# Kernel tuning notes

Hardware: AMD Instinct MI355X
Metric: run time of the kernel (lower is better)

## Reference

```python
import jax, jax.numpy as jnp
import numpy as np

D_MODEL = 1024
NUM_HEADS = 16
D_K = D_MODEL // NUM_HEADS


def setup_inputs() -> dict:
    key = jax.random.key(0)
    ks = jax.random.split(key, 5)
    x = jax.random.normal(ks[0], (8, 1024, D_MODEL), dtype=jnp.float32)
    s_in = 1.0 / np.sqrt(D_MODEL)
    W_qkv = jax.random.normal(ks[1], (D_MODEL, 3 * D_MODEL), dtype=jnp.float32) * s_in
    b_qkv = jax.random.normal(ks[2], (3 * D_MODEL,), dtype=jnp.float32) * 0.01
    W_o = jax.random.normal(ks[3], (D_MODEL, D_MODEL), dtype=jnp.float32) * s_in
    b_o = jax.random.normal(ks[4], (D_MODEL,), dtype=jnp.float32) * 0.01
    return {"x": x, "W_qkv": W_qkv, "b_qkv": b_qkv, "W_o": W_o, "b_o": b_o}


def reference(x, W_qkv, b_qkv, W_o, b_o):
    B, N, D = x.shape
    qkv = x @ W_qkv + b_qkv                      # [B, N, 3D]
    qkv = qkv.reshape(B, N, 3, NUM_HEADS, D_K)
    qkv = jnp.transpose(qkv, (2, 0, 3, 1, 4))    # [3, B, H, N, d_k]
    q, k, v = qkv[0], qkv[1], qkv[2]
    scale = 1.0 / np.sqrt(D_K).astype(np.float32)
    attn = jnp.einsum('bhqd,bhkd->bhqk', q, k) * scale
    attn = jax.nn.softmax(attn, axis=-1)
    out = jnp.einsum('bhqk,bhkd->bhqd', attn, v)  # [B, H, N, d_k]
    out = jnp.transpose(out, (0, 2, 1, 3)).reshape(B, N, D)
    return out @ W_o + b_o
```

## Files before the change

kernel.cpp:

```cpp
#include <hip/hip_runtime.h>


typedef __attribute__((ext_vector_type(8))) short bf16x8;
typedef __attribute__((ext_vector_type(4))) float f32x4;

#define GLOAD_LDS16(gp, lp)                                                              \
  __builtin_amdgcn_global_load_lds((const __attribute__((address_space(1))) void*)(gp),  \
                                   (__attribute__((address_space(3))) void*)(lp), 16, 0, 0)

__device__ __forceinline__ unsigned short f2bf(float f) {
  unsigned int u = __float_as_uint(f);
  u += 0x7fffu + ((u >> 16) & 1u);
  return (unsigned short)(u >> 16);
}

__global__ __launch_bounds__(256) void prep_fused(
    const float* __restrict__ x, unsigned short* __restrict__ x_bf,
    const float* __restrict__ W_qkv, unsigned short* __restrict__ wqkv_t,
    const float* __restrict__ W_o, unsigned short* __restrict__ wo_t) {
  const int b = blockIdx.x;
  if (b < 2048) {
    const int n4 = 8388608 / 4;
    for (int i = b * 256 + threadIdx.x; i < n4; i += 2048 * 256) {
      float4 v = reinterpret_cast<const float4*>(x)[i];
      ushort4 o;
      o.x = f2bf(v.x); o.y = f2bf(v.y); o.z = f2bf(v.z); o.w = f2bf(v.w);
      reinterpret_cast<ushort4*>(x_bf)[i] = o;
    }
  } else {
    __shared__ float tile[32][33];
    const float* W;
    unsigned short* Wt;
    int R = 1024, C, bx, by;
    if (b < 5120) {
      W = W_qkv; Wt = wqkv_t; C = 3072;
      int bb = b - 2048; bx = bb % 96; by = bb / 96;
    } else {
      W = W_o; Wt = wo_t; C = 1024;
      int bb = b - 5120; bx = bb & 31; by = bb >> 5;
    }
    const int tx = threadIdx.x & 31, ty = threadIdx.x >> 5;
    const int c0 = bx * 32, r0 = by * 32;
    #pragma unroll
    for (int i = 0; i < 4; i++) {
      int r = r0 + ty + i * 8;
      tile[ty + i * 8][tx] = W[(size_t)r * C + c0 + tx];
    }
    __syncthreads();
    #pragma unroll
    for (int i = 0; i < 4; i++) {
      int c = c0 + ty + i * 8;
      Wt[(size_t)c * R + r0 + tx] = f2bf(tile[tx][ty + i * 8]);
    }
  }
}

__global__ __launch_bounds__(512) void gemm1_384(
    const unsigned short* __restrict__ A, const unsigned short* __restrict__ Bt,
    const float* __restrict__ bias, unsigned short* __restrict__ qkv_out) {
  __shared__ __align__(16) unsigned short As[3][128 * 32];
  __shared__ __align__(16) unsigned short Bs[3][384 * 32];
  const int t = threadIdx.x;
  const int lane = t & 63, wid = t >> 6;
  const int lr = lane & 15, g = lane >> 4;
  const int wm = wid >> 2, wn = wid & 3;

  const int nwg = gridDim.x * gridDim.y;
  const int id = blockIdx.x + gridDim.x * blockIdx.y;
  const int sw = (id & 7) * (nwg >> 3) + (id >> 3);
  const int bx = sw % gridDim.x, by = sw / gridDim.x;
  const int row0 = by * 128, col0 = bx * 384;

  const int srow = t >> 2;
  const int sch  = (t & 3) ^ ((srow >> 1) & 3);

  auto stA = [&](int buf, int kt) {
    GLOAD_LDS16(A + (size_t)(row0 + srow) * 1024 + kt * 32 + sch * 8,
                (char*)&As[buf][0] + t * 16);
  };
  auto stB = [&](int buf, int kt, int j) {
    GLOAD_LDS16(Bt + (size_t)(col0 + j * 128 + srow) * 1024 + kt * 32 + sch * 8,
                (char*)&Bs[buf][0] + j * 8192 + t * 16);
  };
  auto rdA = [&](int buf, int m) -> bf16x8 {
    int r = wm * 64 + m * 16 + lr;
    return *(const bf16x8*)((const char*)&As[buf][0] + r * 64 +
                            ((g ^ ((r >> 1) & 3)) * 16));
  };
  auto rdB = [&](int buf, int n) -> bf16x8 {
    int r = wn * 96 + n * 16 + lr;
    return *(const bf16x8*)((const char*)&Bs[buf][0] + r * 64 +
                            ((g ^ ((r >> 1) & 3)) * 16));
  };

  f32x4 acc[4][6] = {};

  stA(0, 0); stB(0, 0, 0); stB(0, 0, 1); stB(0, 0, 2);
  stA(1, 1); stB(1, 1, 0); stB(1, 1, 1); stB(1, 1, 2);

  for (int kt = 0; kt < 32; kt++) {
    const int buf = kt % 3;
    const int bufn = (kt + 2) % 3;
    const bool pf = (kt <= 29);

    if (kt == 31) asm volatile("s_waitcnt vmcnt(0)" ::: "memory");
    else          asm volatile("s_waitcnt vmcnt(4)" ::: "memory");
    __builtin_amdgcn_s_barrier();
    __builtin_amdgcn_sched_barrier(0);

    bf16x8 a[4], b[6];
    #pragma unroll
    for (int m = 0; m < 4; m++) a[m] = rdA(buf, m);
    #pragma unroll
    for (int n = 0; n < 6; n++) b[n] = rdB(buf, n);
    if (pf) { stA(bufn, kt + 2); stB(bufn, kt + 2, 0); stB(bufn, kt + 2, 1); stB(bufn, kt + 2, 2); }
    #pragma unroll
    for (int m = 0; m < 4; m++)
      #pragma unroll
      for (int n = 0; n < 6; n++)
        acc[m][n] = __builtin_amdgcn_mfma_f32_16x16x32_bf16(a[m], b[n], acc[m][n], 0, 0, 0);
  }

  #pragma unroll
  for (int m = 0; m < 4; m++) {
    const int row = row0 + wm * 64 + m * 16 + g * 4;
    const int bb = row >> 10, nn = row & 1023;
    #pragma unroll
    for (int n = 0; n < 6; n++) {
      const int col = col0 + wn * 96 + n * 16 + lr;
      const int which = col >> 10;
      const int cc = col & 1023;
      const int h = cc >> 6, dk = cc & 63;
      const float bv = bias[col];
      if (which == 2) {
        ushort4 w;
        w.x = f2bf(acc[m][n][0] + bv);
        w.y = f2bf(acc[m][n][1] + bv);
        w.z = f2bf(acc[m][n][2] + bv);
        w.w = f2bf(acc[m][n][3] + bv);
        size_t idx = ((size_t)2 << 23) + (((size_t)(bb * 16 + h)) << 16) +
                     (size_t)dk * 1024 + nn;
        *(ushort4*)(qkv_out + idx) = w;
      } else {
        const float sc = (which == 0) ? 0.125f : 1.0f;
        #pragma unroll
        for (int r = 0; r < 4; r++) {
          size_t idx = ((size_t)which << 23) +
                       (((size_t)((bb * 16 + h) * 1024 + nn + r)) << 6) + dk;
          qkv_out[idx] = f2bf((acc[m][n][r] + bv) * sc);
        }
      }
    }
  }
}

__global__ __launch_bounds__(512) void gemm2_k(
    const unsigned short* __restrict__ A, const unsigned short* __restrict__ Bt,
    const float* __restrict__ bias, float* __restrict__ Cout) {
  __shared__ __align__(16) unsigned short As[3][128 * 64];
  __shared__ __align__(16) unsigned short Bs[3][256 * 64];
  const int t = threadIdx.x;
  const int lane = t & 63, wid = t >> 6;
  const int lr = lane & 15, g = lane >> 4;
  const int wm = wid >> 2, wn = wid & 3;

  const int nwg = gridDim.x * gridDim.y;
  const int id = blockIdx.x + gridDim.x * blockIdx.y;
  const int sw = (id & 7) * (nwg >> 3) + (id >> 3);
  const int bx = sw % gridDim.x, by = sw / gridDim.x;
  const int row0 = by * 128, col0 = bx * 256;

  const int srow = t >> 3, sch = t & 7;

  auto stA = [&](int buf, int kt, int j) {
    int row = j * 64 + srow;
    int ch = sch ^ (row & 7);
    GLOAD_LDS16(A + (size_t)(row0 + row) * 1024 + kt * 64 + ch * 8,
                (char*)&As[buf][0] + j * 8192 + t * 16);
  };
  auto stB = [&](int buf, int kt, int j) {
    int row = j * 64 + srow;
    int ch = sch ^ (row & 7);
    GLOAD_LDS16(Bt + (size_t)(col0 + row) * 1024 + kt * 64 + ch * 8,
                (char*)&Bs[buf][0] + j * 8192 + t * 16);
  };
  auto rdA = [&](int buf, int c, int m) -> bf16x8 {
    int r = wm * 64 + m * 16 + lr;
    return *(const bf16x8*)((const char*)&As[buf][0] + r * 128 +
                            ((c * 64 + g * 16) ^ ((r & 7) << 4)));
  };
  auto rdB = [&](int buf, int c, int n) -> bf16x8 {
    int r = wn * 64 + n * 16 + lr;
    return *(const bf16x8*)((const char*)&Bs[buf][0] + r * 128 +
                            ((c * 64 + g * 16) ^ ((r & 7) << 4)));
  };

  f32x4 acc[4][4] = {};

  stA(0, 0, 0); stA(0, 0, 1);
  stB(0, 0, 0); stB(0, 0, 1); stB(0, 0, 2); stB(0, 0, 3);
  stA(1, 1, 0); stA(1, 1, 1);
  stB(1, 1, 0); stB(1, 1, 1); stB(1, 1, 2); stB(1, 1, 3);

  for (int kt = 0; kt < 16; kt++) {
    const int buf = kt % 3;
    const int bufn = (kt + 2) % 3;
    const bool pf = (kt <= 13);

    if (kt == 15) asm volatile("s_waitcnt vmcnt(0)" ::: "memory");
    else          asm volatile("s_waitcnt vmcnt(6)" ::: "memory");
    __builtin_amdgcn_s_barrier();
    __builtin_amdgcn_sched_barrier(0);

    bf16x8 a0[4], b0[4];
    #pragma unroll
    for (int m = 0; m < 4; m++) a0[m] = rdA(buf, 0, m);
    #pragma unroll
    for (int n = 0; n < 4; n++) b0[n] = rdB(buf, 0, n);
    if (pf) { stA(bufn, kt + 2, 0); stA(bufn, kt + 2, 1); stB(bufn, kt + 2, 0); }
    #pragma unroll
    for (int m = 0; m < 4; m++)
      #pragma unroll
      for (int n = 0; n < 4; n++)
        acc[m][n] = __builtin_amdgcn_mfma_f32_16x16x32_bf16(a0[m], b0[n], acc[m][n], 0, 0, 0);

    bf16x8 a1[4], b1[4];
    #pragma unroll
    for (int m = 0; m < 4; m++) a1[m] = rdA(buf, 1, m);
    #pragma unroll
    for (int n = 0; n < 4; n++) b1[n] = rdB(buf, 1, n);
    if (pf) { stB(bufn, kt + 2, 1); stB(bufn, kt + 2, 2); stB(bufn, kt + 2, 3); }
    #pragma unroll
    for (int m = 0; m < 4; m++)
      #pragma unroll
      for (int n = 0; n < 4; n++)
        acc[m][n] = __builtin_amdgcn_mfma_f32_16x16x32_bf16(a1[m], b1[n], acc[m][n], 0, 0, 0);
  }

  #pragma unroll
  for (int m = 0; m < 4; m++) {
    #pragma unroll
    for (int n = 0; n < 4; n++) {
      int col = col0 + wn * 64 + n * 16 + lr;
      #pragma unroll
      for (int r = 0; r < 4; r++) {
        int row = row0 + wm * 64 + m * 16 + g * 4 + r;
        Cout[(size_t)row * 1024 + col] = acc[m][n][r] + bias[col];
      }
    }
  }
}

__global__ __launch_bounds__(512) void attn_mfma(
    const unsigned short* __restrict__ qkv, unsigned short* __restrict__ attn_out) {
  __shared__ __align__(16) unsigned short K_lds[2][64 * 64];
  __shared__ __align__(16) unsigned short V_lds[2][64 * 64];
  __shared__ __align__(16) unsigned short P_lds[128 * 64];

  const int bid = ((blockIdx.x & 7) << 7) + (blockIdx.x >> 3);
  const int bh = bid >> 3, qt = bid & 7;
  const unsigned short* Qp = qkv + ((size_t)bh << 16);
  const unsigned short* Kp = qkv + (1u << 23) + ((size_t)bh << 16);
  const unsigned short* Vt = qkv + (2u << 23) + ((size_t)bh << 16);

  const int t = threadIdx.x;
  const int lane = t & 63, wid = t >> 6;
  const int lr = lane & 15, g = lane >> 4;

  bf16x8 qf[2];
  {
    int qrow = qt * 128 + wid * 16 + lr;
    qf[0] = *(const bf16x8*)(Qp + (size_t)qrow * 64 + g * 8);
    qf[1] = *(const bf16x8*)(Qp + (size_t)qrow * 64 + 32 + g * 8);
  }

  const int srow = t >> 3;
  const int sch  = (t & 7) ^ (srow & 7);
  const int so   = t * 16;

  auto stage = [&](int buf, int kt) {
    GLOAD_LDS16(Kp + (size_t)(kt * 64 + srow) * 64 + sch * 8, (char*)&K_lds[buf][0] + so);
    GLOAD_LDS16(Vt + (size_t)srow * 1024 + kt * 64 + sch * 8, (char*)&V_lds[buf][0] + so);
  };

  f32x4 o_acc[4] = {};
  float den_l = 0.f;
  const int qrow_w = wid * 16 + lr;

  stage(0, 0);
  __syncthreads();
  int buf = 0;
  for (int kt = 0; kt < 16; kt++) {
    if (kt + 1 < 16) stage(buf ^ 1, kt + 1);

    f32x4 s4[4] = {};
    __builtin_amdgcn_s_setprio(1);
    #pragma unroll
    for (int ks = 0; ks < 4; ks++) {
      int krow = ks * 16 + lr;
      #pragma unroll
      for (int c = 0; c < 2; c++) {
        bf16x8 kf = *(const bf16x8*)((char*)&K_lds[buf][0] + krow * 128 +
                                     ((c * 64 + g * 16) ^ ((krow & 7) << 4)));
        s4[ks] = __builtin_amdgcn_mfma_f32_16x16x32_bf16(kf, qf[c], s4[ks], 0, 0, 0);
      }
    }
    __builtin_amdgcn_s_setprio(0);

    #pragma unroll
    for (int ks = 0; ks < 4; ks++) {
      float e0 = __expf(s4[ks][0]);
      float e1 = __expf(s4[ks][1]);
      float e2 = __expf(s4[ks][2]);
      float e3 = __expf(s4[ks][3]);
      den_l += (e0 + e1) + (e2 + e3);
      unsigned int lo = (unsigned int)f2bf(e0) | ((unsigned int)f2bf(e1) << 16);
      unsigned int hi = (unsigned int)f2bf(e2) | ((unsigned int)f2bf(e3) << 16);
      int k0 = ks * 16 + g * 4;
      *(uint2*)((char*)P_lds + qrow_w * 128 +
                ((k0 * 2) ^ ((qrow_w & 7) << 4))) = make_uint2(lo, hi);
    }

    bf16x8 pa[2];
    {
      int q = wid * 16 + lr;
      #pragma unroll
      for (int c = 0; c < 2; c++)
        pa[c] = *(const bf16x8*)((char*)P_lds + q * 128 +
                                 ((c * 64 + g * 16) ^ ((q & 7) << 4)));
    }
    __builtin_amdgcn_s_setprio(1);
    #pragma unroll
    for (int ds_ = 0; ds_ < 4; ds_++) {
      int drow = ds_ * 16 + lr;
      #pragma unroll
      for (int c = 0; c < 2; c++) {
        bf16x8 vf = *(const bf16x8*)((char*)&V_lds[buf][0] + drow * 128 +
                                     ((c * 64 + g * 16) ^ ((drow & 7) << 4)));
        o_acc[ds_] = __builtin_amdgcn_mfma_f32_16x16x32_bf16(pa[c], vf, o_acc[ds_], 0, 0, 0);
      }
    }
    __builtin_amdgcn_s_setprio(0);
    __syncthreads();
    buf ^= 1;
  }

  den_l += __shfl_xor(den_l, 16, 64);
  den_l += __shfl_xor(den_l, 32, 64);
  float den_r[4];
  #pragma unroll
  for (int r = 0; r < 4; r++) den_r[r] = __shfl(den_l, g * 4 + r, 64);

  const int bb = bh >> 4, h = bh & 15;
  #pragma unroll
  for (int ds_ = 0; ds_ < 4; ds_++) {
    #pragma unroll
    for (int r = 0; r < 4; r++) {
      int q = qt * 128 + wid * 16 + g * 4 + r;
      int d = h * 64 + ds_ * 16 + lr;
      attn_out[((size_t)(bb * 1024 + q)) * 1024 + d] = f2bf(o_acc[ds_][r] / den_r[r]);
    }
  }
}

extern "C" void kernel_launch(void* const* d_in, const int* in_sizes, int n_in,
                              void* d_out, int out_size, void* d_ws, size_t ws_size,
                              hipStream_t stream) {
  const float* x     = (const float*)d_in[0];
  const float* W_qkv = (const float*)d_in[1];
  const float* b_qkv = (const float*)d_in[2];
  const float* W_o   = (const float*)d_in[3];
  const float* b_o   = (const float*)d_in[4];
  float* out = (float*)d_out;

  unsigned short* ws      = (unsigned short*)d_ws;
  unsigned short* x_bf    = ws;
  unsigned short* wqkv_t  = x_bf + 8388608;
  unsigned short* wo_t    = wqkv_t + 3145728;
  unsigned short* qkv     = wo_t + 1048576;
  unsigned short* attn_o  = qkv + 25165824;

  prep_fused<<<6144, 256, 0, stream>>>(x, x_bf, W_qkv, wqkv_t, W_o, wo_t);
  gemm1_384<<<dim3(8, 64), 512, 0, stream>>>(x_bf, wqkv_t, b_qkv, qkv);
  attn_mfma<<<1024, 512, 0, stream>>>(qkv, attn_o);
  gemm2_k<<<dim3(4, 64), 512, 0, stream>>>(attn_o, wo_t, b_o, out);
}
```

Before: 153.4 us.

## Triple-buffer K/V staging and pass P via lane shuffles instead of LDS

Moves the attention kernel from double to triple buffering of K/V tiles, prefetching two tiles ahead. It replaces __syncthreads with explicit vmcnt waits plus raw barriers. It also drops the P_lds round-trip by rearranging the softmax probabilities into MFMA A-operand layout with cross-lane shuffles. An occupancy hint is added to launch bounds. The goal is to hide global load latency and remove LDS traffic and sync for P, at the cost of more shuffle instructions and more LDS for the extra K/V buffers.

```diff
diff --git a/kernel.cpp b/kernel.cpp
--- a/kernel.cpp
+++ b/kernel.cpp
@@ -251,11 +251,10 @@
   }
 }
 
-__global__ __launch_bounds__(512) void attn_mfma(
+__global__ __launch_bounds__(512, 6) void attn_mfma(
     const unsigned short* __restrict__ qkv, unsigned short* __restrict__ attn_out) {
-  __shared__ __align__(16) unsigned short K_lds[2][64 * 64];
-  __shared__ __align__(16) unsigned short V_lds[2][64 * 64];
-  __shared__ __align__(16) unsigned short P_lds[128 * 64];
+  __shared__ __align__(16) unsigned short K_lds[3][64 * 64];
+  __shared__ __align__(16) unsigned short V_lds[3][64 * 64];
 
   const int bid = ((blockIdx.x & 7) << 7) + (blockIdx.x >> 3);
   const int bh = bid >> 3, qt = bid & 7;
@@ -285,13 +284,16 @@
 
   f32x4 o_acc[4] = {};
   float den_l = 0.f;
-  const int qrow_w = wid * 16 + lr;
-
-  stage(0, 0);
-  __syncthreads();
-  int buf = 0;
+  const bool lo_half = (lane < 32);
+  const bool godd = (g & 1) != 0;
+
+  stage(0, 0); stage(1, 1);
+  asm volatile("s_waitcnt vmcnt(2)" ::: "memory");
+  __builtin_amdgcn_s_barrier();
+
   for (int kt = 0; kt < 16; kt++) {
-    if (kt + 1 < 16) stage(buf ^ 1, kt + 1);
+    const int buf = kt % 3;
+    if (kt + 2 < 16) stage((kt + 2) % 3, kt + 2);
 
     f32x4 s4[4] = {};
     __builtin_amdgcn_s_setprio(1);
@@ -307,6 +309,7 @@
     }
     __builtin_amdgcn_s_setprio(0);
 
+    unsigned int wv[4][2];
     #pragma unroll
     for (int ks = 0; ks < 4; ks++) {
       float e0 = __expf(s4[ks][0]);
@@ -314,21 +317,34 @@
       float e2 = __expf(s4[ks][2]);
       float e3 = __expf(s4[ks][3]);
       den_l += (e0 + e1) + (e2 + e3);
-      unsigned int lo = (unsigned int)f2bf(e0) | ((unsigned int)f2bf(e1) << 16);
-      unsigned int hi = (unsigned int)f2bf(e2) | ((unsigned int)f2bf(e3) << 16);
-      int k0 = ks * 16 + g * 4;
-      *(uint2*)((char*)P_lds + qrow_w * 128 +
-                ((k0 * 2) ^ ((qrow_w & 7) << 4))) = make_uint2(lo, hi);
-    }
-
+      wv[ks][0] = (unsigned int)f2bf(e0) | ((unsigned int)f2bf(e1) << 16);
+      wv[ks][1] = (unsigned int)f2bf(e2) | ((unsigned int)f2bf(e3) << 16);
+    }
+
+    unsigned int paw[2][4];
+    #pragma unroll
+    for (int j = 0; j < 4; j++) {
+      unsigned int a = wv[(j >> 1) * 2][j & 1];
+      unsigned int b = wv[(j >> 1) * 2 + 1][j & 1];
+      unsigned int ax = (unsigned int)__shfl_xor((int)a, 32, 64);
+      unsigned int bx = (unsigned int)__shfl_xor((int)b, 32, 64);
+      unsigned int r0 = lo_half ? a : bx;
+      unsigned int r1 = lo_half ? ax : b;
+      unsigned int s0 = (unsigned int)__shfl_xor((int)r0, 16, 64);
+      unsigned int s1 = (unsigned int)__shfl_xor((int)r1, 16, 64);
+      const int c = j >> 1, i = j & 1;
+      paw[c][i]     = godd ? s1 : r0;
+      paw[c][2 + i] = godd ? r1 : s0;
+    }
     bf16x8 pa[2];
-    {
-      int q = wid * 16 + lr;
-      #pragma unroll
-      for (int c = 0; c < 2; c++)
-        pa[c] = *(const bf16x8*)((char*)P_lds + q * 128 +
-                                 ((c * 64 + g * 16) ^ ((q & 7) << 4)));
-    }
+    #pragma unroll
+    for (int c = 0; c < 2; c++) {
+      union { bf16x8 v; unsigned int u[4]; } cv;
+      cv.u[0] = paw[c][0]; cv.u[1] = paw[c][1];
+      cv.u[2] = paw[c][2]; cv.u[3] = paw[c][3];
+      pa[c] = cv.v;
+    }
+
     __builtin_amdgcn_s_setprio(1);
     #pragma unroll
     for (int ds_ = 0; ds_ < 4; ds_++) {
@@ -341,8 +357,13 @@
       }
     }
     __builtin_amdgcn_s_setprio(0);
-    __syncthreads();
-    buf ^= 1;
+
+    if (kt <= 13)      asm volatile("s_waitcnt vmcnt(2)" ::: "memory");
+    else if (kt == 14) asm volatile("s_waitcnt vmcnt(0)" ::: "memory");
+    if (kt < 15) {
+      __builtin_amdgcn_s_barrier();
+      __builtin_amdgcn_sched_barrier(0);
+    }
   }
 
   den_l += __shfl_xor(den_l, 16, 64);
```

After: 161.0 us. 1.05x slower.
